# Kernel optimization log

Measured on AMD Instinct MI355X. Metric: run time of the kernel, lower is better.

Reference implementation:

```python
import jax, jax.numpy as jnp
import numpy as np

B, N, DIM = 64, 197, 768
NUM_HEAD, HEAD_DIM = 12, 64
SCALE = HEAD_DIM ** -0.5
WS = (14, 14)
NUM_REL = (2 * WS[0] - 1) * (2 * WS[1] - 1) + 3  # 732


def _relative_position_index():
    coords = np.stack(np.meshgrid(np.arange(WS[0]), np.arange(WS[1]), indexing='ij'))  # (2, Wh, Ww)
    cf = coords.reshape(2, -1)                              # (2, Wh*Ww)
    rel = (cf[:, :, None] - cf[:, None, :]).transpose(1, 2, 0).astype(np.int64)
    rel[:, :, 0] += WS[0] - 1
    rel[:, :, 1] += WS[1] - 1
    rel[:, :, 0] *= 2 * WS[1] - 1
    idx = np.zeros((WS[0] * WS[1] + 1,) * 2, dtype=np.int32)
    idx[1:, 1:] = rel.sum(-1)
    idx[0, :] = NUM_REL - 3
    idx[:, 0] = NUM_REL - 2
    idx[0, 0] = NUM_REL - 1
    return idx


def setup_inputs() -> dict:
    key = jax.random.key(0)
    k1, k2, k3, k4 = jax.random.split(key, 4)
    x = jax.random.normal(k1, (B, N, DIM), dtype=jnp.float32)
    qkv_w = jax.random.normal(k2, (3 * DIM, DIM), dtype=jnp.float32) * (DIM ** -0.5)
    q_bias = jnp.zeros((DIM,), dtype=jnp.float32)
    v_bias = jnp.zeros((DIM,), dtype=jnp.float32)
    rpb_table = jax.random.normal(k3, (NUM_REL, NUM_HEAD), dtype=jnp.float32) * 0.02
    proj_w = jax.random.normal(k4, (DIM, DIM), dtype=jnp.float32) * (DIM ** -0.5)
    proj_b = jnp.zeros((DIM,), dtype=jnp.float32)
    rel_index = jnp.asarray(_relative_position_index())
    return {"x": x, "qkv_w": qkv_w, "q_bias": q_bias, "v_bias": v_bias,
            "rpb_table": rpb_table, "proj_w": proj_w, "proj_b": proj_b,
            "rel_index": rel_index}


def reference(x, qkv_w, q_bias, v_bias, rpb_table, proj_w, proj_b, rel_index):
    b, n, c = x.shape
    # qkv projection with [q_bias, 0, v_bias] bias layout
    qkv_bias = jnp.concatenate([q_bias, jnp.zeros_like(v_bias), v_bias])
    qkv = x @ qkv_w.T + qkv_bias                               # (B, N, 3*C)
    qkv = qkv.reshape(b, n, 3, NUM_HEAD, HEAD_DIM).transpose(2, 0, 3, 1, 4)
    q, k, v = qkv[0] * SCALE, qkv[1], qkv[2]                   # (B, H, N, hd)
    attn = jnp.einsum('bhqd,bhkd->bhqk', q, k)                 # (B, H, N, N)
    # relative position bias gather: table[(N,N)] -> (N, N, H) -> (H, N, N)
    bias = rpb_table[rel_index].transpose(2, 0, 1)
    attn = jax.nn.softmax(attn + bias[None], axis=-1)
    out = jnp.einsum('bhqk,bhkd->bhqd', attn, v)               # (B, H, N, hd)
    out = out.transpose(0, 2, 1, 3).reshape(b, n, -1)
    return out @ proj_w.T + proj_b
```

## Files before the change

### kernel.cpp

```cpp
#include <hip/hip_runtime.h>


#define B_    64
#define N_    197
#define DIM_  768
#define H_    12
#define HD_   64
#define M_TOT (B_ * N_)

#define ST_A0   0
#define ST_A1   13312
#define ST_A2   26624
#define ST_B0   39936
#define ST_B1   52224
#define ST_B2   64512
#define OFF_Q   0
#define OFF_K   13312
#define OFF_VT  26624
#define LDS_TOT 76800

typedef __attribute__((ext_vector_type(8))) short bf8;
typedef __attribute__((ext_vector_type(4))) float f4;
typedef __attribute__((ext_vector_type(4))) unsigned short us4;

__device__ __forceinline__ unsigned short f2bf(float f) {
    unsigned u = __float_as_uint(f);
    u = (u + 0x7fffu + ((u >> 16) & 1u)) >> 16;
    return (unsigned short)u;
}
__device__ __forceinline__ float bf2f(unsigned short u) {
    return __uint_as_float((unsigned)u << 16);
}

__device__ __forceinline__ void gl2lds16(const unsigned short* g, unsigned short* l) {
    __builtin_amdgcn_global_load_lds(
        (const __attribute__((address_space(1))) void*)g,
        (__attribute__((address_space(3))) void*)l, 16, 0, 0);
}

__device__ __forceinline__ int qkaddr(int row, int col) {
    return row * 64 + ((((col >> 3) ^ row) & 7) << 3) + (col & 7);
}
__device__ __forceinline__ int vtaddr(int d, int k) {
    int s = k >> 3;
    int s2 = (s < 24) ? ((s & 24) | ((s ^ d) & 7)) : (24 + ((s ^ d) & 3));
    return d * 224 + (s2 << 3) + (k & 7);
}

__global__ void k_prep(const float* __restrict__ x, const float* __restrict__ qkvw,
                       const float* __restrict__ projw, const float* __restrict__ rpb,
                       const int* __restrict__ relidx,
                       unsigned short* __restrict__ x_bf, unsigned short* __restrict__ qkvw_bf,
                       unsigned short* __restrict__ projw_bf,
                       unsigned short* __restrict__ bias_bf) {
    const int T = gridDim.x * blockDim.x;
    const int tid = blockIdx.x * blockDim.x + threadIdx.x;
    for (int i = tid; i < M_TOT * DIM_ / 4; i += T) {
        float4 v = ((const float4*)x)[i];
        us4 o = {f2bf(v.x), f2bf(v.y), f2bf(v.z), f2bf(v.w)};
        ((us4*)x_bf)[i] = o;
    }
    for (int i = tid; i < 3 * DIM_ * DIM_ / 4; i += T) {
        float4 v = ((const float4*)qkvw)[i];
        us4 o = {f2bf(v.x), f2bf(v.y), f2bf(v.z), f2bf(v.w)};
        ((us4*)qkvw_bf)[i] = o;
    }
    for (int i = tid; i < DIM_ * DIM_ / 4; i += T) {
        float4 v = ((const float4*)projw)[i];
        us4 o = {f2bf(v.x), f2bf(v.y), f2bf(v.z), f2bf(v.w)};
        ((us4*)projw_bf)[i] = o;
    }
    for (int i = tid; i < H_ * N_ * 208; i += T) {
        int h = i / (N_ * 208);
        int rem = i - h * (N_ * 208);
        int q = rem / 208, k = rem - (rem / 208) * 208;
        bias_bf[i] = (k < N_) ? f2bf(rpb[relidx[q * N_ + k] * H_ + h])
                              : (unsigned short)0xFF80;
    }
}

__global__ __launch_bounds__(1024) void k_fused(const unsigned short* __restrict__ X,
                                                const unsigned short* __restrict__ Wqkv,
                                                const float* __restrict__ qb,
                                                const float* __restrict__ vbias,
                                                const unsigned short* __restrict__ bias_bf,
                                                unsigned short* __restrict__ att_ws) {
    __shared__ unsigned short lds[LDS_TOT];

    const int t = threadIdx.x;
    const int w = t >> 6, lane = t & 63, ln = lane & 15, quad = lane >> 4;
    const int wm = w >> 2, wn = w & 3;
    const int srl = lane >> 3;
    const int src8 = (lane & 7) ^ srl;

    const int gid = blockIdx.x;
    const int local = gid >> 3;
    const int b = (gid & 7) * 8 + (local & 7);
    const int h = local >> 3;

    const unsigned short* xb = X + (size_t)b * 197 * 768;

    auto stage = [&](int kt, int aOfs, int bOfs) {
#pragma unroll
        for (int i = 0; i < 4; ++i) {
            int idx = (15 - w) + 16 * i;
            if (idx >= 50) break;
            if (idx < 26) {
                int tok = 8 * idx + srl;
                if (tok > 196) tok = 196;
                gl2lds16(xb + (size_t)tok * 768 + kt * 64 + src8 * 8,
                         &lds[aOfs + idx * 512]);
            } else {
                int bb = idx - 26;
                int rr = 8 * bb + srl;
                gl2lds16(Wqkv + (size_t)((rr >> 6) * 768 + h * 64 + (rr & 63)) * 768
                              + kt * 64 + src8 * 8,
                         &lds[bOfs + bb * 512]);
            }
        }
    };

    f4 acc[4][3] = {};

    auto compute = [&](int aOfs, int bOfs) {
#pragma unroll
        for (int ks = 0; ks < 2; ++ks) {
            bf8 bfr[3];
#pragma unroll
            for (int tl = 0; tl < 3; ++tl) {
                int rr = (wn * 3 + tl) * 16 + ln;
                int slot = (ks * 4 + quad) ^ (rr & 7);
                bfr[tl] = *(const bf8*)&lds[bOfs + rr * 64 + slot * 8];
            }
            __builtin_amdgcn_s_setprio(1);
#pragma unroll
            for (int mi = 0; mi < 4; ++mi) {
                int mt = wm + 4 * mi;
                if (mt >= 13) continue;
                int row = mt * 16 + ln;
                int slot = (ks * 4 + quad) ^ (row & 7);
                bf8 af = *(const bf8*)&lds[aOfs + row * 64 + slot * 8];
#pragma unroll
                for (int tl = 0; tl < 3; ++tl)
                    acc[mi][tl] = __builtin_amdgcn_mfma_f32_16x16x32_bf16(
                        af, bfr[tl], acc[mi][tl], 0, 0, 0);
            }
            __builtin_amdgcn_s_setprio(0);
        }
    };

    const int stA[3] = {ST_A0, ST_A1, ST_A2};
    const int stB[3] = {ST_B0, ST_B1, ST_B2};
    stage(0, ST_A0, ST_B0);
    stage(1, ST_A1, ST_B1);
#pragma unroll
    for (int kt = 0; kt < 12; ++kt) {
        if (kt < 11) { __asm__ __volatile__("s_waitcnt vmcnt(3)" ::: "memory"); }
        else         { __asm__ __volatile__("s_waitcnt vmcnt(0)" ::: "memory"); }
        __builtin_amdgcn_sched_barrier(0);
        __builtin_amdgcn_s_barrier();
        __builtin_amdgcn_sched_barrier(0);
        if (kt + 2 < 12) stage(kt + 2, stA[(kt + 2) % 3], stB[(kt + 2) % 3]);
        compute(stA[kt % 3], stB[kt % 3]);
    }
    __syncthreads();

#pragma unroll
    for (int tl = 0; tl < 3; ++tl) {
        int tn = wn * 3 + tl;
        int p = tn >> 2;
        int col = (tn & 3) * 16 + ln;
        int d = h * 64 + col;
        float bj = (p == 0) ? qb[d] : (p == 2) ? vbias[d] : 0.0f;
#pragma unroll
        for (int mi = 0; mi < 4; ++mi) {
            int mt = wm + 4 * mi;
            if (mt >= 13) continue;
#pragma unroll
            for (int r = 0; r < 4; ++r) {
                int row = mt * 16 + quad * 4 + r;
                float v = acc[mi][tl][r];
                if (p == 0)      lds[OFF_Q + qkaddr(row, col)] = f2bf((v + bj) * 0.125f);
                else if (p == 1) lds[OFF_K + qkaddr(row, col)] = f2bf(v);
                else             lds[OFF_VT + vtaddr(col, row)] = f2bf(v + bj);
            }
        }
    }
    for (int idx = t; idx < 64 * 16; idx += 1024) {
        int d = idx >> 4, k = 208 + (idx & 15);
        lds[OFF_VT + vtaddr(d, k)] = 0;
    }
    __syncthreads();

    const unsigned short* bp = bias_bf + (size_t)h * 197 * 208;

    for (int mt = w; mt < 13; mt += 16) {
        bf8 qa[2];
#pragma unroll
        for (int ks = 0; ks < 2; ++ks)
            qa[ks] = *(const bf8*)&lds[OFF_Q + qkaddr(mt * 16 + ln, ks * 32 + quad * 8)];

        int qg = mt * 16 + ln;
        const unsigned short* brow = bp + (size_t)(qg < 197 ? qg : 196) * 208;
        f4 sacc[13];
#pragma unroll
        for (int nt = 0; nt < 13; ++nt) {
            us4 bq = *(const us4*)&brow[nt * 16 + quad * 4];
            sacc[nt] = (f4){bf2f(bq[0]), bf2f(bq[1]), bf2f(bq[2]), bf2f(bq[3])};
        }
        __builtin_amdgcn_s_setprio(1);
#pragma unroll
        for (int nt = 0; nt < 13; ++nt) {
#pragma unroll
            for (int ks = 0; ks < 2; ++ks) {
                bf8 ka = *(const bf8*)&lds[OFF_K + qkaddr(nt * 16 + ln, ks * 32 + quad * 8)];
                sacc[nt] = __builtin_amdgcn_mfma_f32_16x16x32_bf16(ka, qa[ks], sacc[nt], 0, 0, 0);
            }
        }
        __builtin_amdgcn_s_setprio(0);

        float mx = -3.0e38f;
#pragma unroll
        for (int nt = 0; nt < 13; ++nt)
#pragma unroll
            for (int r = 0; r < 4; ++r)
                mx = fmaxf(mx, sacc[nt][r]);
        mx = fmaxf(mx, __shfl_xor(mx, 16, 64));
        mx = fmaxf(mx, __shfl_xor(mx, 32, 64));
        float sum = 0.f;
#pragma unroll
        for (int nt = 0; nt < 13; ++nt)
#pragma unroll
            for (int r = 0; r < 4; ++r) {
                float pv = __expf(sacc[nt][r] - mx);
                sacc[nt][r] = pv;
                sum += pv;
            }
        sum += __shfl_xor(sum, 16, 64);
        sum += __shfl_xor(sum, 32, 64);
        float inv = 1.0f / sum;

        unsigned pk[14][2];
#pragma unroll
        for (int nt = 0; nt < 13; ++nt) {
            pk[nt][0] = (unsigned)f2bf(sacc[nt][0]) |
                        ((unsigned)f2bf(sacc[nt][1]) << 16);
            pk[nt][1] = (unsigned)f2bf(sacc[nt][2]) |
                        ((unsigned)f2bf(sacc[nt][3]) << 16);
        }
        pk[13][0] = 0; pk[13][1] = 0;

        float invq[4];
#pragma unroll
        for (int r = 0; r < 4; ++r) invq[r] = __shfl(inv, quad * 4 + r, 64);

        const int sA = (((lane & 15) | ((lane & 16) << 1)) << 2);
        const int sB = sA + 64;
        const bool hi = (lane & 32) != 0;
        f4 o[4];
#pragma unroll
        for (int j = 0; j < 4; ++j) o[j] = (f4){0.f, 0.f, 0.f, 0.f};
#pragma unroll
        for (int ks = 0; ks < 7; ++ks) {
            int b0 = __builtin_amdgcn_ds_bpermute(sA, (int)pk[2 * ks][0]);
            int b1 = __builtin_amdgcn_ds_bpermute(sA, (int)pk[2 * ks][1]);
            int b2 = __builtin_amdgcn_ds_bpermute(sB, (int)pk[2 * ks][0]);
            int b3 = __builtin_amdgcn_ds_bpermute(sB, (int)pk[2 * ks][1]);
            int c0 = __builtin_amdgcn_ds_bpermute(sA, (int)pk[2 * ks + 1][0]);
            int c1 = __builtin_amdgcn_ds_bpermute(sA, (int)pk[2 * ks + 1][1]);
            int c2 = __builtin_amdgcn_ds_bpermute(sB, (int)pk[2 * ks + 1][0]);
            int c3 = __builtin_amdgcn_ds_bpermute(sB, (int)pk[2 * ks + 1][1]);
            union { int u[4]; bf8 v; } uu;
            uu.u[0] = hi ? c0 : b0;
            uu.u[1] = hi ? c1 : b1;
            uu.u[2] = hi ? c2 : b2;
            uu.u[3] = hi ? c3 : b3;
            __builtin_amdgcn_s_setprio(1);
#pragma unroll
            for (int j = 0; j < 4; ++j) {
                bf8 vf = *(const bf8*)&lds[OFF_VT + vtaddr(j * 16 + ln, ks * 32 + quad * 8)];
                o[j] = __builtin_amdgcn_mfma_f32_16x16x32_bf16(uu.v, vf, o[j], 0, 0, 0);
            }
            __builtin_amdgcn_s_setprio(0);
        }
#pragma unroll
        for (int j = 0; j < 4; ++j)
#pragma unroll
            for (int r = 0; r < 4; ++r) {
                int tok = mt * 16 + quad * 4 + r;
                if (tok < 197)
                    att_ws[((size_t)b * 197 + tok) * 768 + h * 64 + j * 16 + ln]
                        = f2bf(o[j][r] * invq[r]);
            }
    }
}

#define PJ_BUF 8192

__device__ __forceinline__ void pj_stage(const unsigned short* __restrict__ A,
                                         const unsigned short* __restrict__ Bm,
                                         int bm, int bn, int kt, int w, int srl, int src8,
                                         unsigned short* buf) {
#pragma unroll
    for (int i = 0; i < 2; ++i) {
        int idx = w * 2 + i;
        int gr = bm * 128 + 2 * (idx * 8 + srl) + (src8 >> 2);
        if (gr > M_TOT - 1) gr = M_TOT - 1;
        gl2lds16(A + (size_t)gr * 768 + kt * 32 + (src8 & 3) * 8,
                 &buf[idx * 512]);
        int gc = bn * 128 + 2 * (idx * 8 + srl) + (src8 >> 2);
        gl2lds16(Bm + (size_t)gc * 768 + kt * 32 + (src8 & 3) * 8,
                 &buf[4096 + idx * 512]);
    }
}

__device__ __forceinline__ void pj_compute(const unsigned short* buf,
                                           int wm, int wn, int ln, int quad, f4 (*acc)[4]) {
    bf8 af[4], bfr[4];
#pragma unroll
    for (int i = 0; i < 4; ++i) {
        int row = wm * 64 + i * 16 + ln;
        int sr = row >> 1;
        int slot = (((row & 1) << 2) | quad) ^ (sr & 7);
        af[i] = *(const bf8*)&buf[sr * 64 + slot * 8];
    }
#pragma unroll
    for (int j = 0; j < 4; ++j) {
        int row = wn * 64 + j * 16 + ln;
        int sr = row >> 1;
        int slot = (((row & 1) << 2) | quad) ^ (sr & 7);
        bfr[j] = *(const bf8*)&buf[4096 + sr * 64 + slot * 8];
    }
    __builtin_amdgcn_s_setprio(1);
#pragma unroll
    for (int i = 0; i < 4; ++i)
#pragma unroll
        for (int j = 0; j < 4; ++j)
            acc[i][j] = __builtin_amdgcn_mfma_f32_16x16x32_bf16(af[i], bfr[j], acc[i][j], 0, 0, 0);
    __builtin_amdgcn_s_setprio(0);
}

__global__ __launch_bounds__(256, 3) void k_proj(const unsigned short* __restrict__ A,
                                                 const unsigned short* __restrict__ Bm,
                                                 const float* __restrict__ pb,
                                                 float* __restrict__ out) {
    __shared__ unsigned short plds[3 * PJ_BUF];
    const int t = threadIdx.x;
    const int w = t >> 6, lane = t & 63, ln = lane & 15, quad = lane >> 4;
    const int wm = w & 1, wn = w >> 1;

    const int gid = blockIdx.x;
    const int panel = gid / 48, rem = gid - panel * 48;
    const int pm0 = panel * 8;
    const int psz = (99 - pm0 < 8) ? (99 - pm0) : 8;
    const int bm = pm0 + rem % psz;
    const int bn = rem / psz;

    const int srl = lane >> 3;
    const int src8 = (lane & 7) ^ srl;

    f4 acc[4][4] = {};

    pj_stage(A, Bm, bm, bn, 0, w, srl, src8, &plds[0]);
    pj_stage(A, Bm, bm, bn, 1, w, srl, src8, &plds[PJ_BUF]);
#pragma unroll
    for (int kt = 0; kt < 24; ++kt) {
        if (kt < 23) { __asm__ __volatile__("s_waitcnt vmcnt(4)" ::: "memory"); }
        else         { __asm__ __volatile__("s_waitcnt vmcnt(0)" ::: "memory"); }
        __builtin_amdgcn_sched_barrier(0);
        __builtin_amdgcn_s_barrier();
        __builtin_amdgcn_sched_barrier(0);
        if (kt + 2 < 24) pj_stage(A, Bm, bm, bn, kt + 2, w, srl, src8,
                                  &plds[((kt + 2) % 3) * PJ_BUF]);
        pj_compute(&plds[(kt % 3) * PJ_BUF], wm, wn, ln, quad, acc);
    }

#pragma unroll
    for (int i = 0; i < 4; ++i) {
#pragma unroll
        for (int r = 0; r < 4; ++r) {
            int row_g = bm * 128 + wm * 64 + i * 16 + quad * 4 + r;
            if (row_g >= M_TOT) continue;
#pragma unroll
            for (int j = 0; j < 4; ++j) {
                int col_g = bn * 128 + wn * 64 + j * 16 + ln;
                out[(size_t)row_g * 768 + col_g] = acc[i][j][r] + pb[col_g];
            }
        }
    }
}

extern "C" void kernel_launch(void* const* d_in, const int* in_sizes, int n_in,
                              void* d_out, int out_size, void* d_ws, size_t ws_size,
                              hipStream_t stream) {
    const float* x     = (const float*)d_in[0];
    const float* qkvw  = (const float*)d_in[1];
    const float* qb    = (const float*)d_in[2];
    const float* vb    = (const float*)d_in[3];
    const float* rpb   = (const float*)d_in[4];
    const float* projw = (const float*)d_in[5];
    const float* pb    = (const float*)d_in[6];
    const int*   ridx  = (const int*)d_in[7];
    float* out = (float*)d_out;

    char* ws = (char*)d_ws;
    size_t off = 0;
    auto alloc = [&](size_t bytes) -> void* {
        void* p = ws + off;
        off = (off + bytes + 255) & ~(size_t)255;
        return p;
    };
    unsigned short* x_bf     = (unsigned short*)alloc((size_t)M_TOT * DIM_ * 2);
    unsigned short* qkvw_bf  = (unsigned short*)alloc((size_t)3 * DIM_ * DIM_ * 2);
    unsigned short* projw_bf = (unsigned short*)alloc((size_t)DIM_ * DIM_ * 2);
    unsigned short* bias_bf  = (unsigned short*)alloc((size_t)H_ * N_ * 208 * 2);
    unsigned short* att_ws   = (unsigned short*)alloc((size_t)(M_TOT + 64) * DIM_ * 2);
    (void)ws_size; (void)in_sizes; (void)n_in; (void)out_size;

    k_prep<<<1200, 256, 0, stream>>>(x, qkvw, projw, rpb, ridx,
                                     x_bf, qkvw_bf, projw_bf, bias_bf);
    k_fused<<<768, 1024, 0, stream>>>(x_bf, qkvw_bf, qb, vb, bias_bf, att_ws);
    k_proj<<<594, 256, 0, stream>>>(att_ws, projw_bf, pb, out);
}
```

Measured before the change: 203.8 us.

## Make fused attention kernel persistent over three heads with overlapped prefetch

The fused QKV+attention kernel now launches 256 blocks instead of 768, and each block loops over three heads (h0, h0+4, h0+8). The staging tile shrinks from K=64 to K=32 per step, with a new swizzle, so Q/K/V scratch fits next to the triple buffer in LDS. While the attention phase of one head runs, the first two tiles for the next head's projection are prefetched, hiding the pipeline prologue. The cost is less parallelism across the GPU (256 blocks of 1024 threads), twice as many barrier steps per head, and slightly more LDS per block.

```diff
diff --git a/kernel.cpp b/kernel.cpp
--- a/kernel.cpp
+++ b/kernel.cpp
@@ -8,16 +8,11 @@
 #define HD_   64
 #define M_TOT (B_ * N_)
 
-#define ST_A0   0
-#define ST_A1   13312
-#define ST_A2   26624
-#define ST_B0   39936
-#define ST_B1   52224
-#define ST_B2   64512
-#define OFF_Q   0
-#define OFF_K   13312
-#define OFF_VT  26624
-#define LDS_TOT 76800
+#define ST_BUF  12800
+#define OFF_Q   38400
+#define OFF_K   51712
+#define OFF_VT  65024
+#define LDS_TOT 79360
 
 typedef __attribute__((ext_vector_type(8))) short bf8;
 typedef __attribute__((ext_vector_type(4))) float f4;
@@ -96,41 +91,48 @@
     const int gid = blockIdx.x;
     const int local = gid >> 3;
     const int b = (gid & 7) * 8 + (local & 7);
-    const int h = local >> 3;
+    const int h0 = local >> 3;
 
     const unsigned short* xb = X + (size_t)b * 197 * 768;
 
-    auto stage = [&](int kt, int aOfs, int bOfs) {
-#pragma unroll
-        for (int i = 0; i < 4; ++i) {
+    auto stage = [&](int h, int kt, int bufi) {
+        int aOfs = bufi * ST_BUF, bOfs = aOfs + 6656;
+#pragma unroll
+        for (int i = 0; i < 2; ++i) {
             int idx = (15 - w) + 16 * i;
-            if (idx >= 50) break;
-            if (idx < 26) {
-                int tok = 8 * idx + srl;
+            if (idx >= 25) break;
+            if (idx < 13) {
+                int tok = 2 * (idx * 8 + srl) + (src8 >> 2);
                 if (tok > 196) tok = 196;
-                gl2lds16(xb + (size_t)tok * 768 + kt * 64 + src8 * 8,
+                gl2lds16(xb + (size_t)tok * 768 + kt * 32 + (src8 & 3) * 8,
                          &lds[aOfs + idx * 512]);
             } else {
-                int bb = idx - 26;
-                int rr = 8 * bb + srl;
+                int bb = idx - 13;
+                int rr = 2 * (bb * 8 + srl) + (src8 >> 2);
                 gl2lds16(Wqkv + (size_t)((rr >> 6) * 768 + h * 64 + (rr & 63)) * 768
-                              + kt * 64 + src8 * 8,
+                              + kt * 32 + (src8 & 3) * 8,
                          &lds[bOfs + bb * 512]);
             }
         }
     };
 
-    f4 acc[4][3] = {};
-
-    auto compute = [&](int aOfs, int bOfs) {
-#pragma unroll
-        for (int ks = 0; ks < 2; ++ks) {
+    stage(h0, 0, 0);
+    stage(h0, 1, 1);
+
+    for (int pi = 0; pi < 3; ++pi) {
+        const int h = h0 + 4 * pi;
+
+        f4 acc[4][3] = {};
+
+        auto compute = [&](int bufi) {
+            int aOfs = bufi * ST_BUF, bOfs = aOfs + 6656;
             bf8 bfr[3];
 #pragma unroll
             for (int tl = 0; tl < 3; ++tl) {
                 int rr = (wn * 3 + tl) * 16 + ln;
-                int slot = (ks * 4 + quad) ^ (rr & 7);
-                bfr[tl] = *(const bf8*)&lds[bOfs + rr * 64 + slot * 8];
+                int sr = rr >> 1;
+                int slot = (((rr & 1) << 2) | quad) ^ (sr & 7);
+                bfr[tl] = *(const bf8*)&lds[bOfs + sr * 64 + slot * 8];
             }
             __builtin_amdgcn_s_setprio(1);
 #pragma unroll
@@ -138,160 +140,165 @@
                 int mt = wm + 4 * mi;
                 if (mt >= 13) continue;
                 int row = mt * 16 + ln;
-                int slot = (ks * 4 + quad) ^ (row & 7);
-                bf8 af = *(const bf8*)&lds[aOfs + row * 64 + slot * 8];
+                int sr = row >> 1;
+                int slot = (((row & 1) << 2) | quad) ^ (sr & 7);
+                bf8 af = *(const bf8*)&lds[aOfs + sr * 64 + slot * 8];
 #pragma unroll
                 for (int tl = 0; tl < 3; ++tl)
                     acc[mi][tl] = __builtin_amdgcn_mfma_f32_16x16x32_bf16(
                         af, bfr[tl], acc[mi][tl], 0, 0, 0);
             }
             __builtin_amdgcn_s_setprio(0);
-        }
-    };
-
-    const int stA[3] = {ST_A0, ST_A1, ST_A2};
-    const int stB[3] = {ST_B0, ST_B1, ST_B2};
-    stage(0, ST_A0, ST_B0);
-    stage(1, ST_A1, ST_B1);
-#pragma unroll
-    for (int kt = 0; kt < 12; ++kt) {
-        if (kt < 11) { __asm__ __volatile__("s_waitcnt vmcnt(3)" ::: "memory"); }
-        else         { __asm__ __volatile__("s_waitcnt vmcnt(0)" ::: "memory"); }
-        __builtin_amdgcn_sched_barrier(0);
-        __builtin_amdgcn_s_barrier();
-        __builtin_amdgcn_sched_barrier(0);
-        if (kt + 2 < 12) stage(kt + 2, stA[(kt + 2) % 3], stB[(kt + 2) % 3]);
-        compute(stA[kt % 3], stB[kt % 3]);
-    }
-    __syncthreads();
-
-#pragma unroll
-    for (int tl = 0; tl < 3; ++tl) {
-        int tn = wn * 3 + tl;
-        int p = tn >> 2;
-        int col = (tn & 3) * 16 + ln;
-        int d = h * 64 + col;
-        float bj = (p == 0) ? qb[d] : (p == 2) ? vbias[d] : 0.0f;
-#pragma unroll
-        for (int mi = 0; mi < 4; ++mi) {
-            int mt = wm + 4 * mi;
-            if (mt >= 13) continue;
-#pragma unroll
-            for (int r = 0; r < 4; ++r) {
-                int row = mt * 16 + quad * 4 + r;
-                float v = acc[mi][tl][r];
-                if (p == 0)      lds[OFF_Q + qkaddr(row, col)] = f2bf((v + bj) * 0.125f);
-                else if (p == 1) lds[OFF_K + qkaddr(row, col)] = f2bf(v);
-                else             lds[OFF_VT + vtaddr(col, row)] = f2bf(v + bj);
-            }
-        }
-    }
-    for (int idx = t; idx < 64 * 16; idx += 1024) {
-        int d = idx >> 4, k = 208 + (idx & 15);
-        lds[OFF_VT + vtaddr(d, k)] = 0;
-    }
-    __syncthreads();
-
-    const unsigned short* bp = bias_bf + (size_t)h * 197 * 208;
-
-    for (int mt = w; mt < 13; mt += 16) {
-        bf8 qa[2];
-#pragma unroll
-        for (int ks = 0; ks < 2; ++ks)
-            qa[ks] = *(const bf8*)&lds[OFF_Q + qkaddr(mt * 16 + ln, ks * 32 + quad * 8)];
-
-        int qg = mt * 16 + ln;
-        const unsigned short* brow = bp + (size_t)(qg < 197 ? qg : 196) * 208;
-        f4 sacc[13];
-#pragma unroll
-        for (int nt = 0; nt < 13; ++nt) {
-            us4 bq = *(const us4*)&brow[nt * 16 + quad * 4];
-            sacc[nt] = (f4){bf2f(bq[0]), bf2f(bq[1]), bf2f(bq[2]), bf2f(bq[3])};
-        }
-        __builtin_amdgcn_s_setprio(1);
-#pragma unroll
-        for (int nt = 0; nt < 13; ++nt) {
-#pragma unroll
-            for (int ks = 0; ks < 2; ++ks) {
-                bf8 ka = *(const bf8*)&lds[OFF_K + qkaddr(nt * 16 + ln, ks * 32 + quad * 8)];
-                sacc[nt] = __builtin_amdgcn_mfma_f32_16x16x32_bf16(ka, qa[ks], sacc[nt], 0, 0, 0);
-            }
-        }
-        __builtin_amdgcn_s_setprio(0);
-
-        float mx = -3.0e38f;
-#pragma unroll
-        for (int nt = 0; nt < 13; ++nt)
-#pragma unroll
-            for (int r = 0; r < 4; ++r)
-                mx = fmaxf(mx, sacc[nt][r]);
-        mx = fmaxf(mx, __shfl_xor(mx, 16, 64));
-        mx = fmaxf(mx, __shfl_xor(mx, 32, 64));
-        float sum = 0.f;
-#pragma unroll
-        for (int nt = 0; nt < 13; ++nt)
-#pragma unroll
-            for (int r = 0; r < 4; ++r) {
-                float pv = __expf(sacc[nt][r] - mx);
-                sacc[nt][r] = pv;
-                sum += pv;
-            }
-        sum += __shfl_xor(sum, 16, 64);
-        sum += __shfl_xor(sum, 32, 64);
-        float inv = 1.0f / sum;
-
-        unsigned pk[14][2];
-#pragma unroll
-        for (int nt = 0; nt < 13; ++nt) {
-            pk[nt][0] = (unsigned)f2bf(sacc[nt][0]) |
-                        ((unsigned)f2bf(sacc[nt][1]) << 16);
-            pk[nt][1] = (unsigned)f2bf(sacc[nt][2]) |
-                        ((unsigned)f2bf(sacc[nt][3]) << 16);
-        }
-        pk[13][0] = 0; pk[13][1] = 0;
-
-        float invq[4];
-#pragma unroll
-        for (int r = 0; r < 4; ++r) invq[r] = __shfl(inv, quad * 4 + r, 64);
-
-        const int sA = (((lane & 15) | ((lane & 16) << 1)) << 2);
-        const int sB = sA + 64;
-        const bool hi = (lane & 32) != 0;
-        f4 o[4];
-#pragma unroll
-        for (int j = 0; j < 4; ++j) o[j] = (f4){0.f, 0.f, 0.f, 0.f};
-#pragma unroll
-        for (int ks = 0; ks < 7; ++ks) {
-            int b0 = __builtin_amdgcn_ds_bpermute(sA, (int)pk[2 * ks][0]);
-            int b1 = __builtin_amdgcn_ds_bpermute(sA, (int)pk[2 * ks][1]);
-            int b2 = __builtin_amdgcn_ds_bpermute(sB, (int)pk[2 * ks][0]);
-            int b3 = __builtin_amdgcn_ds_bpermute(sB, (int)pk[2 * ks][1]);
-            int c0 = __builtin_amdgcn_ds_bpermute(sA, (int)pk[2 * ks + 1][0]);
-            int c1 = __builtin_amdgcn_ds_bpermute(sA, (int)pk[2 * ks + 1][1]);
-            int c2 = __builtin_amdgcn_ds_bpermute(sB, (int)pk[2 * ks + 1][0]);
-            int c3 = __builtin_amdgcn_ds_bpermute(sB, (int)pk[2 * ks + 1][1]);
-            union { int u[4]; bf8 v; } uu;
-            uu.u[0] = hi ? c0 : b0;
-            uu.u[1] = hi ? c1 : b1;
-            uu.u[2] = hi ? c2 : b2;
-            uu.u[3] = hi ? c3 : b3;
+        };
+
+#pragma unroll
+        for (int kt = 0; kt < 24; ++kt) {
+            if (kt < 23) {
+                if (w >= 7) { __asm__ __volatile__("s_waitcnt vmcnt(2)" ::: "memory"); }
+                else        { __asm__ __volatile__("s_waitcnt vmcnt(1)" ::: "memory"); }
+            } else {
+                __asm__ __volatile__("s_waitcnt vmcnt(0)" ::: "memory");
+            }
+            __builtin_amdgcn_sched_barrier(0);
+            __builtin_amdgcn_s_barrier();
+            __builtin_amdgcn_sched_barrier(0);
+            if (kt + 2 < 24) stage(h, kt + 2, (kt + 2) % 3);
+            compute(kt % 3);
+        }
+
+#pragma unroll
+        for (int tl = 0; tl < 3; ++tl) {
+            int tn = wn * 3 + tl;
+            int p = tn >> 2;
+            int col = (tn & 3) * 16 + ln;
+            int d = h * 64 + col;
+            float bj = (p == 0) ? qb[d] : (p == 2) ? vbias[d] : 0.0f;
+#pragma unroll
+            for (int mi = 0; mi < 4; ++mi) {
+                int mt = wm + 4 * mi;
+                if (mt >= 13) continue;
+#pragma unroll
+                for (int r = 0; r < 4; ++r) {
+                    int row = mt * 16 + quad * 4 + r;
+                    float v = acc[mi][tl][r];
+                    if (p == 0)      lds[OFF_Q + qkaddr(row, col)] = f2bf((v + bj) * 0.125f);
+                    else if (p == 1) lds[OFF_K + qkaddr(row, col)] = f2bf(v);
+                    else             lds[OFF_VT + vtaddr(col, row)] = f2bf(v + bj);
+                }
+            }
+        }
+        for (int idx = t; idx < 64 * 16; idx += 1024) {
+            int d = idx >> 4, k = 208 + (idx & 15);
+            lds[OFF_VT + vtaddr(d, k)] = 0;
+        }
+        __syncthreads();
+
+        if (pi + 1 < 3) {
+            stage(h0 + 4 * (pi + 1), 0, 0);
+            stage(h0 + 4 * (pi + 1), 1, 1);
+        }
+
+        const unsigned short* bp = bias_bf + (size_t)h * 197 * 208;
+
+        for (int mt = w; mt < 13; mt += 16) {
+            bf8 qa[2];
+#pragma unroll
+            for (int ks = 0; ks < 2; ++ks)
+                qa[ks] = *(const bf8*)&lds[OFF_Q + qkaddr(mt * 16 + ln, ks * 32 + quad * 8)];
+
+            int qg = mt * 16 + ln;
+            const unsigned short* brow = bp + (size_t)(qg < 197 ? qg : 196) * 208;
+            f4 sacc[13];
+#pragma unroll
+            for (int nt = 0; nt < 13; ++nt) {
+                us4 bq = *(const us4*)&brow[nt * 16 + quad * 4];
+                sacc[nt] = (f4){bf2f(bq[0]), bf2f(bq[1]), bf2f(bq[2]), bf2f(bq[3])};
+            }
             __builtin_amdgcn_s_setprio(1);
 #pragma unroll
-            for (int j = 0; j < 4; ++j) {
-                bf8 vf = *(const bf8*)&lds[OFF_VT + vtaddr(j * 16 + ln, ks * 32 + quad * 8)];
-                o[j] = __builtin_amdgcn_mfma_f32_16x16x32_bf16(uu.v, vf, o[j], 0, 0, 0);
+            for (int nt = 0; nt < 13; ++nt) {
+#pragma unroll
+                for (int ks = 0; ks < 2; ++ks) {
+                    bf8 ka = *(const bf8*)&lds[OFF_K + qkaddr(nt * 16 + ln, ks * 32 + quad * 8)];
+                    sacc[nt] = __builtin_amdgcn_mfma_f32_16x16x32_bf16(ka, qa[ks], sacc[nt], 0, 0, 0);
+                }
             }
             __builtin_amdgcn_s_setprio(0);
-        }
-#pragma unroll
-        for (int j = 0; j < 4; ++j)
-#pragma unroll
-            for (int r = 0; r < 4; ++r) {
-                int tok = mt * 16 + quad * 4 + r;
-                if (tok < 197)
-                    att_ws[((size_t)b * 197 + tok) * 768 + h * 64 + j * 16 + ln]
-                        = f2bf(o[j][r] * invq[r]);
-            }
+
+            float mx = -3.0e38f;
+#pragma unroll
+            for (int nt = 0; nt < 13; ++nt)
+#pragma unroll
+                for (int r = 0; r < 4; ++r)
+                    mx = fmaxf(mx, sacc[nt][r]);
+            mx = fmaxf(mx, __shfl_xor(mx, 16, 64));
+            mx = fmaxf(mx, __shfl_xor(mx, 32, 64));
+            float sum = 0.f;
+#pragma unroll
+            for (int nt = 0; nt < 13; ++nt)
+#pragma unroll
+                for (int r = 0; r < 4; ++r) {
+                    float pv = __expf(sacc[nt][r] - mx);
+                    sacc[nt][r] = pv;
+                    sum += pv;
+                }
+            sum += __shfl_xor(sum, 16, 64);
+            sum += __shfl_xor(sum, 32, 64);
+            float inv = 1.0f / sum;
+
+            unsigned pk[14][2];
+#pragma unroll
+            for (int nt = 0; nt < 13; ++nt) {
+                pk[nt][0] = (unsigned)f2bf(sacc[nt][0]) |
+                            ((unsigned)f2bf(sacc[nt][1]) << 16);
+                pk[nt][1] = (unsigned)f2bf(sacc[nt][2]) |
+                            ((unsigned)f2bf(sacc[nt][3]) << 16);
+            }
+            pk[13][0] = 0; pk[13][1] = 0;
+
+            float invq[4];
+#pragma unroll
+            for (int r = 0; r < 4; ++r) invq[r] = __shfl(inv, quad * 4 + r, 64);
+
+            const int sA = (((lane & 15) | ((lane & 16) << 1)) << 2);
+            const int sB = sA + 64;
+            const bool hi = (lane & 32) != 0;
+            f4 o[4];
+#pragma unroll
+            for (int j = 0; j < 4; ++j) o[j] = (f4){0.f, 0.f, 0.f, 0.f};
+#pragma unroll
+            for (int ks = 0; ks < 7; ++ks) {
+                int b0 = __builtin_amdgcn_ds_bpermute(sA, (int)pk[2 * ks][0]);
+                int b1 = __builtin_amdgcn_ds_bpermute(sA, (int)pk[2 * ks][1]);
+                int b2 = __builtin_amdgcn_ds_bpermute(sB, (int)pk[2 * ks][0]);
+                int b3 = __builtin_amdgcn_ds_bpermute(sB, (int)pk[2 * ks][1]);
+                int c0 = __builtin_amdgcn_ds_bpermute(sA, (int)pk[2 * ks + 1][0]);
+                int c1 = __builtin_amdgcn_ds_bpermute(sA, (int)pk[2 * ks + 1][1]);
+                int c2 = __builtin_amdgcn_ds_bpermute(sB, (int)pk[2 * ks + 1][0]);
+                int c3 = __builtin_amdgcn_ds_bpermute(sB, (int)pk[2 * ks + 1][1]);
+                union { int u[4]; bf8 v; } uu;
+                uu.u[0] = hi ? c0 : b0;
+                uu.u[1] = hi ? c1 : b1;
+                uu.u[2] = hi ? c2 : b2;
+                uu.u[3] = hi ? c3 : b3;
+                __builtin_amdgcn_s_setprio(1);
+#pragma unroll
+                for (int j = 0; j < 4; ++j) {
+                    bf8 vf = *(const bf8*)&lds[OFF_VT + vtaddr(j * 16 + ln, ks * 32 + quad * 8)];
+                    o[j] = __builtin_amdgcn_mfma_f32_16x16x32_bf16(uu.v, vf, o[j], 0, 0, 0);
+                }
+                __builtin_amdgcn_s_setprio(0);
+            }
+#pragma unroll
+            for (int j = 0; j < 4; ++j)
+#pragma unroll
+                for (int r = 0; r < 4; ++r) {
+                    int tok = mt * 16 + quad * 4 + r;
+                    if (tok < 197)
+                        att_ws[((size_t)b * 197 + tok) * 768 + h * 64 + j * 16 + ln]
+                            = f2bf(o[j][r] * invq[r]);
+                }
+        }
     }
 }
 
@@ -419,6 +426,6 @@
 
     k_prep<<<1200, 256, 0, stream>>>(x, qkvw, projw, rpb, ridx,
                                      x_bf, qkvw_bf, projw_bf, bias_bf);
-    k_fused<<<768, 1024, 0, stream>>>(x_bf, qkvw_bf, qb, vb, bias_bf, att_ws);
+    k_fused<<<256, 1024, 0, stream>>>(x_bf, qkvw_bf, qb, vb, bias_bf, att_ws);
     k_proj<<<594, 256, 0, stream>>>(att_ws, projw_bf, pb, out);
 }
```

Result: slower. 332.5 us (+63.2%).
